# Performance work log

Measured on AMD Instinct MI355X. Metric: run time of the kernel, lower is better.

## Reference

```python
import math
import jax, jax.numpy as jnp
import numpy as np

EMBED_DIM = 1024
NUM_HEADS = 16
HEAD_DIM = EMBED_DIM // NUM_HEADS
ROTARY_DIM = HEAD_DIM  # default: rotary_dim = head_dim
BASE = 10000.0


def _rope_cos_sin(seq_len, d, dtype=jnp.float32):
    # theta: [d/2], positions: [S]
    theta = 1.0 / (BASE ** (jnp.arange(0, d, 2, dtype=jnp.float32) / d))
    pos = jnp.arange(seq_len, dtype=jnp.float32)
    idx_theta = pos[:, None] * theta[None, :]          # [S, d/2]
    idx_theta2 = jnp.concatenate([idx_theta, idx_theta], axis=-1)  # [S, d]
    return jnp.cos(idx_theta2).astype(dtype), jnp.sin(idx_theta2).astype(dtype)


def _apply_rope(x):
    # x: [B, H, S, head_dim]; rotate first ROTARY_DIM features
    S = x.shape[-2]
    cos, sin = _rope_cos_sin(S, ROTARY_DIM, x.dtype)   # [S, ROTARY_DIM]
    x_rope, x_pass = x[..., :ROTARY_DIM], x[..., ROTARY_DIM:]
    d2 = ROTARY_DIM // 2
    neg_half = jnp.concatenate([-x_rope[..., d2:], x_rope[..., :d2]], axis=-1)
    x_rope = x_rope * cos + neg_half * sin
    return jnp.concatenate([x_rope, x_pass], axis=-1)


def setup_inputs() -> dict:
    key = jax.random.key(0)
    ks = jax.random.split(key, 9)
    B, S, E = 4, 2048, EMBED_DIM
    scale = 1.0 / math.sqrt(E)
    inp = {
        "x": jax.random.normal(ks[0], (B, S, E), dtype=jnp.float32),
        "attn_mask": jnp.ones((B, S), dtype=jnp.int32),
        "Wq": jax.random.normal(ks[1], (E, E), dtype=jnp.float32) * scale,
        "bq": jnp.zeros((E,), dtype=jnp.float32),
        "Wk": jax.random.normal(ks[2], (E, E), dtype=jnp.float32) * scale,
        "bk": jnp.zeros((E,), dtype=jnp.float32),
        "Wv": jax.random.normal(ks[3], (E, E), dtype=jnp.float32) * scale,
        "bv": jnp.zeros((E,), dtype=jnp.float32),
        "Wo": jax.random.normal(ks[4], (E, E), dtype=jnp.float32) * scale,
        "bo": jnp.zeros((E,), dtype=jnp.float32),
    }
    return inp


def reference(x, attn_mask, Wq, bq, Wk, bk, Wv, bv, Wo, bo):
    B, S, E = x.shape
    H, D = NUM_HEADS, HEAD_DIM

    def proj(W, b):
        # [B,S,E] -> [B,H,S,D]
        y = jnp.einsum('bse,ef->bsf', x, W) + b
        return y.reshape(B, S, H, D).transpose(0, 2, 1, 3)

    q = _apply_rope(proj(Wq, bq))
    k = _apply_rope(proj(Wk, bk))
    v = proj(Wv, bv)

    scores = jnp.einsum('bhsd,bhtd->bhst', q, k) / math.sqrt(D)  # [B,H,S,S]
    mask = attn_mask[:, None, None, :]  # [B,1,1,S]
    scores = jnp.where(mask == 0, jnp.float32(-1e9).astype(scores.dtype), scores)
    attn = jax.nn.softmax(scores, axis=-1)
    out = jnp.einsum('bhst,bhtd->bhsd', attn, v)  # [B,H,S,D]
    out = out.transpose(0, 2, 1, 3).reshape(B, S, E)
    return jnp.einsum('bse,ef->bsf', out, Wo) + bo
```

## Files before the change

kernel.cpp:

```cpp
#include <hip/hip_runtime.h>
#include <math.h>

typedef __attribute__((ext_vector_type(8))) short short8;
typedef __attribute__((ext_vector_type(4))) float f32x4;
typedef __attribute__((ext_vector_type(4))) unsigned short us4;
typedef __attribute__((ext_vector_type(4))) unsigned int u32x4;
typedef __attribute__((ext_vector_type(4))) int i32x4;
typedef unsigned short u16;
typedef unsigned int u32;

#define LOG2E 1.4426950408889634f

static __device__ __forceinline__ u16 f2bf(float f){
  u32 u = __builtin_bit_cast(u32, f);
  u = (u + 0x7FFFu + ((u >> 16) & 1u)) >> 16;
  return (u16)u;
}

static __device__ __forceinline__ void gload16(const void* g, void* l){
  __builtin_amdgcn_global_load_lds((const __attribute__((address_space(1))) void*)g,
                                   (__attribute__((address_space(3))) void*)l,
                                   16, 0, 0);
}

static __device__ __forceinline__ f32x4 mfma16(short8 a, short8 b, f32x4 c){
  return __builtin_amdgcn_mfma_f32_16x16x32_bf16(a, b, c, 0, 0, 0);
}

__global__ void rope_tab_k(float* __restrict__ cosT, float* __restrict__ sinT){
  int idx = blockIdx.x * 256 + threadIdx.x;
  int s = idx >> 5, i = idx & 31;
  double th = pow(10000.0, -((double)(2 * i)) / 64.0);
  float ang = (float)s * (float)th;
  cosT[idx] = (float)cos((double)ang);
  sinT[idx] = (float)sin((double)ang);
}

__global__ void cvt_x_k(const float* __restrict__ x, u16* __restrict__ xb, int n){
  int i = (blockIdx.x * 256 + threadIdx.x) * 4;
  if (i >= n) return;
  f32x4 v = *(const f32x4*)(x + i);
  us4 o; o[0]=f2bf(v[0]); o[1]=f2bf(v[1]); o[2]=f2bf(v[2]); o[3]=f2bf(v[3]);
  *(us4*)(xb + i) = o;
}

__global__ void wt_cvt_k(const float* __restrict__ W0, const float* __restrict__ W1,
                         const float* __restrict__ W2, const float* __restrict__ W3,
                         u16* __restrict__ out){
  __shared__ float t[32][33];
  const float* W = (blockIdx.z == 0) ? W0 : (blockIdx.z == 1) ? W1 : (blockIdx.z == 2) ? W2 : W3;
  u16* O = out + (size_t)blockIdx.z * 1024 * 1024;
  int tx = threadIdx.x, ty = threadIdx.y;
  int kb = blockIdx.y * 32, nb = blockIdx.x * 32;
  #pragma unroll
  for (int i = 0; i < 4; i++)
    t[ty + i*8][tx] = W[(size_t)(kb + ty + i*8) * 1024 + nb + tx];
  __syncthreads();
  #pragma unroll
  for (int i = 0; i < 4; i++)
    O[(size_t)(nb + ty + i*8) * 1024 + kb + tx] = f2bf(t[tx][ty + i*8]);
}

__global__ __launch_bounds__(256, 2)
void qkv_gemm_k(const u16* __restrict__ A, const u16* __restrict__ WT,
                const float* __restrict__ bq, const float* __restrict__ bk,
                const float* __restrict__ bv,
                const float* __restrict__ cosT, const float* __restrict__ sinT,
                u16* __restrict__ Qr, u16* __restrict__ Kr, u16* __restrict__ Vt)
{
  __shared__ __align__(16) u16 Al[128][64];
  __shared__ __align__(16) u16 Bl[128][64];
  const int mode = blockIdx.y >> 3;
  const int cy   = blockIdx.y & 7;
  const u16* BT = WT + (size_t)mode * 1024 * 1024;
  const float* bias = (mode == 0) ? bq : (mode == 1) ? bk : bv;
  u16* outB = (mode == 0) ? Qr : (mode == 1) ? Kr : Vt;

  const int tid = threadIdx.x;
  const int w = tid >> 6, lane = tid & 63, g = lane >> 4, c = lane & 15;
  const int wr = w >> 1, wc = w & 1;
  const int R0 = blockIdx.x * 128, C0 = cy * 128;

  f32x4 acc[4][4];
  const f32x4 vz = {0.f, 0.f, 0.f, 0.f};
  #pragma unroll
  for (int mi = 0; mi < 4; mi++)
    #pragma unroll
    for (int ni = 0; ni < 4; ni++) acc[mi][ni] = vz;

  const u16* gA[4]; const u16* gB[4]; u16* lA[4]; u16* lB[4];
  #pragma unroll
  for (int i = 0; i < 4; i++){
    int I = w * 4 + i;
    int rr = I * 8 + (lane >> 3), kk = (lane & 7) * 8;
    gA[i] = A  + (size_t)(R0 + rr) * 1024 + kk;
    gB[i] = BT + (size_t)(C0 + rr) * 1024 + kk;
    lA[i] = &Al[I * 8][0];
    lB[i] = &Bl[I * 8][0];
  }

  for (int t = 0; t < 16; ++t){
    const int k0 = t * 64;
    #pragma unroll
    for (int i = 0; i < 4; i++){
      gload16(gA[i] + k0, lA[i]);
      gload16(gB[i] + k0, lB[i]);
    }
    __syncthreads();
    #pragma unroll
    for (int ki = 0; ki < 2; ++ki){
      short8 af[4], bfr[4];
      #pragma unroll
      for (int mi = 0; mi < 4; mi++) af[mi]  = *(const short8*)&Al[wr*64 + mi*16 + c][ki*32 + g*8];
      #pragma unroll
      for (int ni = 0; ni < 4; ni++) bfr[ni] = *(const short8*)&Bl[wc*64 + ni*16 + c][ki*32 + g*8];
      #pragma unroll
      for (int mi = 0; mi < 4; mi++)
        #pragma unroll
        for (int ni = 0; ni < 4; ni++)
          acc[mi][ni] = mfma16(af[mi], bfr[ni], acc[mi][ni]);
    }
    __syncthreads();
  }

  if (mode == 2){
    int h = cy * 2 + wc;
    #pragma unroll
    for (int ni = 0; ni < 4; ni++){
      int col = C0 + wc*64 + ni*16 + c;
      int d = ni*16 + c;
      float bvv = bias[col];
      #pragma unroll
      for (int mi = 0; mi < 4; mi++){
        int row0 = R0 + wr*64 + mi*16 + g*4;
        int b = row0 >> 11, s0 = row0 & 2047;
        us4 pk;
        #pragma unroll
        for (int r = 0; r < 4; r++) pk[r] = f2bf(acc[mi][ni][r] + bvv);
        *(us4*)&outB[((size_t)(b*16 + h)*64 + d)*2048 + s0] = pk;
      }
    }
  } else {
    int h = cy * 2 + wc;
    const float qs = (mode == 0) ? 0.125f : 1.0f;
    float bvv[4];
    #pragma unroll
    for (int ni = 0; ni < 4; ni++) bvv[ni] = bias[C0 + wc*64 + ni*16 + c];
    #pragma unroll
    for (int mi = 0; mi < 4; mi++){
      int row0 = R0 + wr*64 + mi*16 + g*4;
      int b = row0 >> 11;
      #pragma unroll
      for (int r = 0; r < 4; r++){
        int s = (row0 + r) & 2047;
        float v0 = acc[mi][0][r] + bvv[0];
        float v1 = acc[mi][1][r] + bvv[1];
        float v2 = acc[mi][2][r] + bvv[2];
        float v3 = acc[mi][3][r] + bvv[3];
        float ca = cosT[s*32 + c],      sa = sinT[s*32 + c];
        float cb = cosT[s*32 + 16 + c], sb = sinT[s*32 + 16 + c];
        float o0 = (v0*ca - v2*sa) * qs, o2 = (v2*ca + v0*sa) * qs;
        float o1 = (v1*cb - v3*sb) * qs, o3 = (v3*cb + v1*sb) * qs;
        size_t base = ((size_t)(b*16 + h)*2048 + s)*64;
        outB[base +  0 + c] = f2bf(o0);
        outB[base + 16 + c] = f2bf(o1);
        outB[base + 32 + c] = f2bf(o2);
        outB[base + 48 + c] = f2bf(o3);
      }
    }
  }
}

__global__ __launch_bounds__(256, 2)
void out_gemm_k(const u16* __restrict__ A, const u16* __restrict__ BT,
                const float* __restrict__ bias, float* __restrict__ outF)
{
  __shared__ __align__(16) u16 Al[128][64];
  __shared__ __align__(16) u16 Bl[128][64];
  const int tid = threadIdx.x;
  const int w = tid >> 6, lane = tid & 63, g = lane >> 4, c = lane & 15;
  const int wr = w >> 1, wc = w & 1;
  const int R0 = blockIdx.x * 128, C0 = blockIdx.y * 128;

  f32x4 acc[4][4];
  const f32x4 vz = {0.f, 0.f, 0.f, 0.f};
  #pragma unroll
  for (int mi = 0; mi < 4; mi++)
    #pragma unroll
    for (int ni = 0; ni < 4; ni++) acc[mi][ni] = vz;

  const u16* gA[4]; const u16* gB[4]; u16* lA[4]; u16* lB[4];
  #pragma unroll
  for (int i = 0; i < 4; i++){
    int I = w * 4 + i;
    int rr = I * 8 + (lane >> 3), kk = (lane & 7) * 8;
    gA[i] = A  + (size_t)(R0 + rr) * 1024 + kk;
    gB[i] = BT + (size_t)(C0 + rr) * 1024 + kk;
    lA[i] = &Al[I * 8][0];
    lB[i] = &Bl[I * 8][0];
  }

  for (int t = 0; t < 16; ++t){
    const int k0 = t * 64;
    #pragma unroll
    for (int i = 0; i < 4; i++){
      gload16(gA[i] + k0, lA[i]);
      gload16(gB[i] + k0, lB[i]);
    }
    __syncthreads();
    #pragma unroll
    for (int ki = 0; ki < 2; ++ki){
      short8 af[4], bfr[4];
      #pragma unroll
      for (int mi = 0; mi < 4; mi++) af[mi]  = *(const short8*)&Al[wr*64 + mi*16 + c][ki*32 + g*8];
      #pragma unroll
      for (int ni = 0; ni < 4; ni++) bfr[ni] = *(const short8*)&Bl[wc*64 + ni*16 + c][ki*32 + g*8];
      #pragma unroll
      for (int mi = 0; mi < 4; mi++)
        #pragma unroll
        for (int ni = 0; ni < 4; ni++)
          acc[mi][ni] = mfma16(af[mi], bfr[ni], acc[mi][ni]);
    }
    __syncthreads();
  }

  #pragma unroll
  for (int mi = 0; mi < 4; mi++){
    #pragma unroll
    for (int ni = 0; ni < 4; ni++){
      int col = C0 + wc*64 + ni*16 + c;
      float bvv = bias[col];
      int row0 = R0 + wr*64 + mi*16 + g*4;
      #pragma unroll
      for (int r = 0; r < 4; r++)
        outF[(size_t)(row0 + r) * 1024 + col] = acc[mi][ni][r] + bvv;
    }
  }
}

__global__ __launch_bounds__(512, 4)
void attn_fwd_k(const u16* __restrict__ Q, const u16* __restrict__ K, const u16* __restrict__ V,
                const int* __restrict__ msk, u16* __restrict__ AO)
{
  __shared__ __align__(16) u16 Kl[4][64][64];
  __shared__ __align__(16) u16 Vl[4][64][64];
  __shared__ __align__(8) unsigned char Ml[2048];
  const int tid = threadIdx.x;
  const int w = tid >> 6, lane = tid & 63, g = lane >> 4, c = lane & 15;

  const int lin = blockIdx.y * 8 + blockIdx.x;
  const int v_  = (lin & 7) * 64 + (lin >> 3);
  const int bh = v_ >> 3, b = bh >> 4, h = bh & 15;
  const int qw = (v_ & 7) * 256 + w * 32;

  {
    const int* mp = msk + b*2048 + tid*4;
    i32x4 a = *(const i32x4*)mp;
    u32 lo = (a[0] ? 1u : 0u) | (a[1] ? 0x100u : 0u) | (a[2] ? 0x10000u : 0u) | (a[3] ? 0x1000000u : 0u);
    *(u32*)&Ml[tid*4] = lo;
  }
  asm volatile("s_waitcnt lgkmcnt(0)" ::: "memory");

  short8 qb[2][2];
  #pragma unroll
  for (int mq = 0; mq < 2; mq++)
    #pragma unroll
    for (int ki = 0; ki < 2; ki++)
      qb[mq][ki] = *(const short8*)&Q[((size_t)bh*2048 + qw + mq*16 + c)*64 + ki*32 + g*8];

  const int l3 = lane >> 3, l7 = lane & 7;
  const int scol = (l7 ^ l3) * 8;
  const int s8 = w*8 + l3;
  const int ps = (s8 & 0x20) | ((s8 & 0x10) >> 2) | ((s8 & 0x0C) << 1) | (s8 & 3);
  const u16* gK = K + ((size_t)bh*2048 + ps)*64 + scol;
  const u16* gV = V + ((size_t)bh*64 + s8)*2048 + scol;

  gload16(gK,                       &Kl[0][w*8][0]);
  gload16(gV,                       &Vl[0][w*8][0]);
  gload16(gK + (size_t)64*64,       &Kl[1][w*8][0]);
  gload16(gV + (size_t)64,          &Vl[1][w*8][0]);

  f32x4 oacc[2][4];
  float mrun[2], lrun[2];
  const f32x4 vz = {0.f, 0.f, 0.f, 0.f};
  #pragma unroll
  for (int mq = 0; mq < 2; mq++){
    #pragma unroll
    for (int nd = 0; nd < 4; nd++) oacc[mq][nd] = vz;
    mrun[mq] = -1e30f; lrun[mq] = 0.f;
  }

  const int cs0 = (g*8) ^ ((c & 7) << 3);
  const int cs1 = (32 + g*8) ^ ((c & 7) << 3);

  for (int t = 0; t < 32; ++t){
    gload16(gK + (size_t)(t+2) * 64 * 64, &Kl[(t+2)&3][w*8][0]);
    gload16(gV + (size_t)(t+2) * 64,      &Vl[(t+2)&3][w*8][0]);
    asm volatile("s_waitcnt vmcnt(4)" ::: "memory");
    __builtin_amdgcn_s_barrier();
    asm volatile("" ::: "memory");

    const u16* Kb = &Kl[t&3][0][0];
    const u16* Vb = &Vl[t&3][0][0];
    const int t0 = t * 64;

    f32x4 sacc[4][2];
    #pragma unroll
    for (int nt = 0; nt < 4; nt++){ sacc[nt][0] = vz; sacc[nt][1] = vz; }
    #pragma unroll
    for (int ki = 0; ki < 2; ki++){
      const int cs = ki ? cs1 : cs0;
      short8 ka[4];
      #pragma unroll
      for (int nt = 0; nt < 4; nt++) ka[nt] = *(const short8*)&Kb[(nt*16 + c)*64 + cs];
      __builtin_amdgcn_s_setprio(1);
      #pragma unroll
      for (int nt = 0; nt < 4; nt++)
        #pragma unroll
        for (int mq = 0; mq < 2; mq++)
          sacc[nt][mq] = mfma16(ka[nt], qb[mq][ki], sacc[nt][mq]);
      __builtin_amdgcn_s_setprio(0);
    }

    {
      const u32 mw0 = *(const u32*)&Ml[t0 + 8*g];
      const u32 mw1 = *(const u32*)&Ml[t0 + 8*g + 4];
      const u32 mw2 = *(const u32*)&Ml[t0 + 32 + 8*g];
      const u32 mw3 = *(const u32*)&Ml[t0 + 32 + 8*g + 4];
      if (!__all((mw0 & mw1 & mw2 & mw3) == 0x01010101u)){
        const u32 mw[4] = {mw0, mw1, mw2, mw3};
        #pragma unroll
        for (int nt = 0; nt < 4; nt++)
          #pragma unroll
          for (int r = 0; r < 4; r++)
            if (((mw[nt] >> (8*r)) & 0xFFu) == 0){ sacc[nt][0][r] = -1e9f; sacc[nt][1][r] = -1e9f; }
      }
    }

    float pm[2];
    #pragma unroll
    for (int mq = 0; mq < 2; mq++){
      float a0 = fmaxf(fmaxf(sacc[0][mq][0], sacc[0][mq][1]), fmaxf(sacc[0][mq][2], sacc[0][mq][3]));
      float a1 = fmaxf(fmaxf(sacc[1][mq][0], sacc[1][mq][1]), fmaxf(sacc[1][mq][2], sacc[1][mq][3]));
      float a2 = fmaxf(fmaxf(sacc[2][mq][0], sacc[2][mq][1]), fmaxf(sacc[2][mq][2], sacc[2][mq][3]));
      float a3 = fmaxf(fmaxf(sacc[3][mq][0], sacc[3][mq][1]), fmaxf(sacc[3][mq][2], sacc[3][mq][3]));
      float mm = fmaxf(fmaxf(a0, a1), fmaxf(a2, a3));
      mm = fmaxf(mm, __shfl_xor(mm, 16, 64));
      mm = fmaxf(mm, __shfl_xor(mm, 32, 64));
      pm[mq] = mm;
    }

    if (__any((pm[0] > mrun[0] + 8.f) | (pm[1] > mrun[1] + 8.f))){
      float al[2];
      #pragma unroll
      for (int mq = 0; mq < 2; mq++){
        float mn = fmaxf(mrun[mq], pm[mq]);
        al[mq] = exp2f((mrun[mq] - mn) * LOG2E);
        mrun[mq] = mn;
        lrun[mq] *= al[mq];
      }
      #pragma unroll
      for (int mq = 0; mq < 2; mq++){
        float b0 = __shfl(al[mq], g*4 + 0, 64);
        float b1 = __shfl(al[mq], g*4 + 1, 64);
        float b2 = __shfl(al[mq], g*4 + 2, 64);
        float b3 = __shfl(al[mq], g*4 + 3, 64);
        #pragma unroll
        for (int nd = 0; nd < 4; nd++){
          oacc[mq][nd][0] *= b0; oacc[mq][nd][1] *= b1;
          oacc[mq][nd][2] *= b2; oacc[mq][nd][3] *= b3;
        }
      }
    }

    short8 pa[2][2];
    #pragma unroll
    for (int mq = 0; mq < 2; mq++){
      const float nm = -mrun[mq] * LOG2E;
      float p[16]; u32 rb[16];
      #pragma unroll
      for (int nt = 0; nt < 4; nt++)
        #pragma unroll
        for (int r = 0; r < 4; r++){
          float pp = exp2f(fmaf(sacc[nt][mq][r], LOG2E, nm));
          p[nt*4 + r] = pp;
          u32 u = __builtin_bit_cast(u32, pp);
          rb[nt*4 + r] = u + 0x7FFFu + ((u >> 16) & 1u);
        }
      float s0 = (p[0] + p[1]) + (p[2] + p[3]);
      float s1 = (p[4] + p[5]) + (p[6] + p[7]);
      float s2 = (p[8] + p[9]) + (p[10] + p[11]);
      float s3 = (p[12] + p[13]) + (p[14] + p[15]);
      lrun[mq] += (s0 + s1) + (s2 + s3);
      u32x4 q0 = { __builtin_amdgcn_perm(rb[1],  rb[0],  0x07060302u),
                   __builtin_amdgcn_perm(rb[3],  rb[2],  0x07060302u),
                   __builtin_amdgcn_perm(rb[5],  rb[4],  0x07060302u),
                   __builtin_amdgcn_perm(rb[7],  rb[6],  0x07060302u) };
      u32x4 q1 = { __builtin_amdgcn_perm(rb[9],  rb[8],  0x07060302u),
                   __builtin_amdgcn_perm(rb[11], rb[10], 0x07060302u),
                   __builtin_amdgcn_perm(rb[13], rb[12], 0x07060302u),
                   __builtin_amdgcn_perm(rb[15], rb[14], 0x07060302u) };
      pa[mq][0] = __builtin_bit_cast(short8, q0);
      pa[mq][1] = __builtin_bit_cast(short8, q1);
    }

    #pragma unroll
    for (int ki = 0; ki < 2; ki++){
      const int cs = ki ? cs1 : cs0;
      short8 va[4];
      #pragma unroll
      for (int nd = 0; nd < 4; nd++) va[nd] = *(const short8*)&Vb[(nd*16 + c)*64 + cs];
      __builtin_amdgcn_s_setprio(1);
      #pragma unroll
      for (int mq = 0; mq < 2; mq++)
        #pragma unroll
        for (int nd = 0; nd < 4; nd++)
          oacc[mq][nd] = mfma16(pa[mq][ki], va[nd], oacc[mq][nd]);
      __builtin_amdgcn_s_setprio(0);
    }
  }

  #pragma unroll
  for (int mq = 0; mq < 2; mq++){
    lrun[mq] += __shfl_xor(lrun[mq], 16, 64);
    lrun[mq] += __shfl_xor(lrun[mq], 32, 64);
    #pragma unroll
    for (int r = 0; r < 4; r++){
      float li = __shfl(lrun[mq], g*4 + r, 64);
      float inv = 1.0f / li;
      int q = qw + mq*16 + g*4 + r;
      size_t base = ((size_t)b*2048 + q)*1024 + h*64;
      #pragma unroll
      for (int nd = 0; nd < 4; nd++)
        AO[base + nd*16 + c] = f2bf(oacc[mq][nd][r] * inv);
    }
  }
}

extern "C" void kernel_launch(void* const* d_in, const int* in_sizes, int n_in,
                              void* d_out, int out_size, void* d_ws, size_t ws_size,
                              hipStream_t stream)
{
  const float* x  = (const float*)d_in[0];
  const int* mask = (const int*)d_in[1];
  const float* Wq = (const float*)d_in[2];
  const float* bq = (const float*)d_in[3];
  const float* Wk = (const float*)d_in[4];
  const float* bk = (const float*)d_in[5];
  const float* Wv = (const float*)d_in[6];
  const float* bv = (const float*)d_in[7];
  const float* Wo = (const float*)d_in[8];
  const float* bo = (const float*)d_in[9];
  float* out = (float*)d_out;
  (void)in_sizes; (void)n_in; (void)out_size; (void)ws_size;

  char* ws = (char*)d_ws;
  size_t off = 0;
  auto alloc = [&](size_t bytes){ void* p = ws + off; off += (bytes + 255) & ~(size_t)255; return p; };
  u16* xb    = (u16*)alloc((size_t)8192 * 1024 * 2);
  u16* WT    = (u16*)alloc((size_t)4 * 1024 * 1024 * 2);
  float* cosT = (float*)alloc((size_t)2048 * 32 * 4);
  float* sinT = (float*)alloc((size_t)2048 * 32 * 4);
  u16* Qr    = (u16*)alloc((size_t)8192 * 1024 * 2);
  u16* Kr    = (u16*)alloc((size_t)8192 * 1024 * 2);
  u16* Vt    = (u16*)alloc((size_t)8192 * 1024 * 2);
  u16* AO    = (u16*)alloc((size_t)8192 * 1024 * 2);

  rope_tab_k<<<dim3(256), dim3(256), 0, stream>>>(cosT, sinT);
  cvt_x_k<<<dim3(8192), dim3(256), 0, stream>>>(x, xb, 8192 * 1024);
  wt_cvt_k<<<dim3(32, 32, 4), dim3(32, 8), 0, stream>>>(Wq, Wk, Wv, Wo, WT);

  qkv_gemm_k<<<dim3(64, 24), dim3(256), 0, stream>>>(xb, WT, bq, bk, bv, cosT, sinT, Qr, Kr, Vt);

  attn_fwd_k<<<dim3(8, 64), dim3(512), 0, stream>>>(Qr, Kr, Vt, mask, AO);

  out_gemm_k<<<dim3(64, 8), dim3(256), 0, stream>>>(AO, WT + 3*1024*1024, bo, out);
}
```

Measured before the change: 242.9 us.

## Rewrite QKV GEMM as 256x256 persistent 8-wave kernel with double-buffered LDS

Replaces the 128x128 single-buffered QKV projection GEMM with a 512-thread, 8-wave kernel computing 256x256 tiles over a persistent grid of 256 blocks. Global-to-LDS loads are double-buffered and interleaved with MFMA phases, using explicit vmcnt waits, barriers and s_setprio, and LDS columns are XOR-swizzled to reduce bank conflicts. The goal is to hide load latency and raise arithmetic intensity per block. The costs are 128KB of LDS per block and larger accumulator register pressure. The 384 tiles do not divide evenly over 256 blocks, so half the blocks do a second tile and the last wave is imbalanced.

```diff
diff --git a/kernel.cpp b/kernel.cpp
--- a/kernel.cpp
+++ b/kernel.cpp
@@ -61,114 +61,157 @@
     O[(size_t)(nb + ty + i*8) * 1024 + kb + tx] = f2bf(t[tx][ty + i*8]);
 }
 
-__global__ __launch_bounds__(256, 2)
-void qkv_gemm_k(const u16* __restrict__ A, const u16* __restrict__ WT,
-                const float* __restrict__ bq, const float* __restrict__ bk,
-                const float* __restrict__ bv,
-                const float* __restrict__ cosT, const float* __restrict__ sinT,
-                u16* __restrict__ Qr, u16* __restrict__ Kr, u16* __restrict__ Vt)
+__global__ __launch_bounds__(512, 2)
+void qkv_gemm8_k(const u16* __restrict__ A, const u16* __restrict__ WT,
+                 const float* __restrict__ bq, const float* __restrict__ bk,
+                 const float* __restrict__ bv,
+                 const float* __restrict__ cosT, const float* __restrict__ sinT,
+                 u16* __restrict__ Qr, u16* __restrict__ Kr, u16* __restrict__ Vt)
 {
-  __shared__ __align__(16) u16 Al[128][64];
-  __shared__ __align__(16) u16 Bl[128][64];
-  const int mode = blockIdx.y >> 3;
-  const int cy   = blockIdx.y & 7;
-  const u16* BT = WT + (size_t)mode * 1024 * 1024;
-  const float* bias = (mode == 0) ? bq : (mode == 1) ? bk : bv;
-  u16* outB = (mode == 0) ? Qr : (mode == 1) ? Kr : Vt;
-
+  __shared__ __align__(16) u16 Al[2][256][64];
+  __shared__ __align__(16) u16 Bl[2][256][64];
   const int tid = threadIdx.x;
   const int w = tid >> 6, lane = tid & 63, g = lane >> 4, c = lane & 15;
-  const int wr = w >> 1, wc = w & 1;
-  const int R0 = blockIdx.x * 128, C0 = cy * 128;
-
-  f32x4 acc[4][4];
-  const f32x4 vz = {0.f, 0.f, 0.f, 0.f};
-  #pragma unroll
-  for (int mi = 0; mi < 4; mi++)
-    #pragma unroll
-    for (int ni = 0; ni < 4; ni++) acc[mi][ni] = vz;
-
-  const u16* gA[4]; const u16* gB[4]; u16* lA[4]; u16* lB[4];
-  #pragma unroll
-  for (int i = 0; i < 4; i++){
-    int I = w * 4 + i;
-    int rr = I * 8 + (lane >> 3), kk = (lane & 7) * 8;
-    gA[i] = A  + (size_t)(R0 + rr) * 1024 + kk;
-    gB[i] = BT + (size_t)(C0 + rr) * 1024 + kk;
-    lA[i] = &Al[I * 8][0];
-    lB[i] = &Bl[I * 8][0];
-  }
-
-  for (int t = 0; t < 16; ++t){
-    const int k0 = t * 64;
-    #pragma unroll
-    for (int i = 0; i < 4; i++){
-      gload16(gA[i] + k0, lA[i]);
-      gload16(gB[i] + k0, lB[i]);
-    }
-    __syncthreads();
-    #pragma unroll
-    for (int ki = 0; ki < 2; ++ki){
-      short8 af[4], bfr[4];
-      #pragma unroll
-      for (int mi = 0; mi < 4; mi++) af[mi]  = *(const short8*)&Al[wr*64 + mi*16 + c][ki*32 + g*8];
-      #pragma unroll
-      for (int ni = 0; ni < 4; ni++) bfr[ni] = *(const short8*)&Bl[wc*64 + ni*16 + c][ki*32 + g*8];
-      #pragma unroll
-      for (int mi = 0; mi < 4; mi++)
-        #pragma unroll
-        for (int ni = 0; ni < 4; ni++)
-          acc[mi][ni] = mfma16(af[mi], bfr[ni], acc[mi][ni]);
-    }
-    __syncthreads();
-  }
-
-  if (mode == 2){
-    int h = cy * 2 + wc;
-    #pragma unroll
-    for (int ni = 0; ni < 4; ni++){
-      int col = C0 + wc*64 + ni*16 + c;
-      int d = ni*16 + c;
-      float bvv = bias[col];
-      #pragma unroll
-      for (int mi = 0; mi < 4; mi++){
-        int row0 = R0 + wr*64 + mi*16 + g*4;
-        int b = row0 >> 11, s0 = row0 & 2047;
-        us4 pk;
-        #pragma unroll
-        for (int r = 0; r < 4; r++) pk[r] = f2bf(acc[mi][ni][r] + bvv);
-        *(us4*)&outB[((size_t)(b*16 + h)*64 + d)*2048 + s0] = pk;
+  const int wm = w >> 2, wn = w & 3;
+  const int l3 = lane >> 3, l7 = lane & 7;
+  const int cswz = ((c >> 2) & 1) << 4;
+
+#define STAGE_A(KT, H) do{ int kt_ = (KT); if (kt_ <= 15){ \
+    _Pragma("unroll") for (int j = 0; j < 2; j++){ \
+      int ib = w*16 + j*8; \
+      int rT = ((ib>>6)<<7) + (H)*64 + (ib & 63); \
+      int row = rT + l3; \
+      int ce = (l7*8) ^ (((row>>2)&1) << 4); \
+      gload16(A + (size_t)(R0 + row)*1024 + kt_*64 + ce, &Al[kt_&1][rT][0]); \
+    }}}while(0)
+
+#define STAGE_B(KT, H) do{ int kt_ = (KT); if (kt_ <= 15){ \
+    _Pragma("unroll") for (int j = 0; j < 2; j++){ \
+      int ib = w*16 + j*8; \
+      int rT = ((ib>>5)<<6) + (H)*32 + (ib & 31); \
+      int row = rT + l3; \
+      int ce = (l7*8) ^ (((row>>2)&1) << 4); \
+      gload16(BT + (size_t)(C0 + row)*1024 + kt_*64 + ce, &Bl[kt_&1][rT][0]); \
+    }}}while(0)
+
+#define RD_A(MH, BUF) do{ _Pragma("unroll") for (int mi = 0; mi < 4; mi++) \
+    _Pragma("unroll") for (int ki = 0; ki < 2; ki++) \
+      af[mi][ki] = *(const short8*)&Al[BUF][wm*128 + (MH)*64 + mi*16 + c][(ki*32 + g*8) ^ cswz]; }while(0)
+
+#define RD_B(DST, NH, BUF) do{ _Pragma("unroll") for (int ni = 0; ni < 2; ni++) \
+    _Pragma("unroll") for (int ki = 0; ki < 2; ki++) \
+      DST[ni][ki] = *(const short8*)&Bl[BUF][wn*64 + (NH)*32 + ni*16 + c][(ki*32 + g*8) ^ cswz]; }while(0)
+
+#define MM(MH, NH, BSRC) do{ __builtin_amdgcn_s_setprio(1); \
+    _Pragma("unroll") for (int ki = 0; ki < 2; ki++) \
+      _Pragma("unroll") for (int mi = 0; mi < 4; mi++) \
+        _Pragma("unroll") for (int ni = 0; ni < 2; ni++) \
+          acc[(MH)*4+mi][(NH)*2+ni] = mfma16(af[mi][ki], BSRC[ni][ki], acc[(MH)*4+mi][(NH)*2+ni]); \
+    __builtin_amdgcn_s_setprio(0); }while(0)
+
+#define BAR() do{ asm volatile("" ::: "memory"); __builtin_amdgcn_s_barrier(); asm volatile("" ::: "memory"); }while(0)
+
+  for (int tile = blockIdx.x; tile < 384; tile += 256){
+    const int rowT = tile & 31, colT = tile >> 5;
+    const int mode = colT >> 2, cy = colT & 3;
+    const int R0 = rowT * 256;
+    const int C0 = cy * 256;
+    const u16* BT = WT + (size_t)mode * 1024 * 1024;
+    const float* bias = (mode == 0) ? bq : (mode == 1) ? bk : bv;
+
+    f32x4 acc[8][4];
+    const f32x4 vz = {0.f, 0.f, 0.f, 0.f};
+    #pragma unroll
+    for (int m = 0; m < 8; m++)
+      #pragma unroll
+      for (int n = 0; n < 4; n++) acc[m][n] = vz;
+
+    short8 af[4][2], bf0[2][2], bf1[2][2];
+
+    STAGE_A(0, 0); STAGE_B(0, 0); STAGE_B(0, 1); STAGE_A(0, 1);
+    STAGE_A(1, 0); STAGE_B(1, 0); STAGE_B(1, 1);
+    asm volatile("s_waitcnt vmcnt(6)" ::: "memory");
+    BAR();
+
+    for (int it = 0; it < 8; ++it){
+      const int T = it * 2;
+      RD_A(0, 0); RD_B(bf0, 0, 0); STAGE_A(T+1, 1);
+      BAR(); MM(0, 0, bf0); BAR();
+      RD_B(bf1, 1, 0); STAGE_A(T+2, 0);
+      BAR(); MM(0, 1, bf1); BAR();
+      RD_A(1, 0); STAGE_B(T+2, 0);
+      BAR(); MM(1, 1, bf1); BAR();
+      STAGE_B(T+2, 1);
+      BAR(); MM(1, 0, bf0);
+      if (it < 7) asm volatile("s_waitcnt vmcnt(6)" ::: "memory");
+      else        asm volatile("s_waitcnt vmcnt(0)" ::: "memory");
+      BAR();
+      RD_A(0, 1); RD_B(bf0, 0, 1); STAGE_A(T+2, 1);
+      BAR(); MM(0, 0, bf0); BAR();
+      RD_B(bf1, 1, 1); STAGE_A(T+3, 0);
+      BAR(); MM(0, 1, bf1); BAR();
+      RD_A(1, 1); STAGE_B(T+3, 0);
+      BAR(); MM(1, 1, bf1); BAR();
+      STAGE_B(T+3, 1);
+      BAR(); MM(1, 0, bf0);
+      if (it < 7) asm volatile("s_waitcnt vmcnt(6)" ::: "memory");
+      else        asm volatile("s_waitcnt vmcnt(0)" ::: "memory");
+      BAR();
+    }
+
+    const int h = cy * 4 + wn;
+    if (mode == 2){
+      #pragma unroll
+      for (int n = 0; n < 4; n++){
+        int d = n*16 + c;
+        float bvv = bias[C0 + wn*64 + n*16 + c];
+        #pragma unroll
+        for (int m = 0; m < 8; m++){
+          int row0 = R0 + wm*128 + m*16 + g*4;
+          int b = row0 >> 11, s0 = row0 & 2047;
+          us4 pk;
+          #pragma unroll
+          for (int r = 0; r < 4; r++) pk[r] = f2bf(acc[m][n][r] + bvv);
+          *(us4*)&Vt[((size_t)(b*16 + h)*64 + d)*2048 + s0] = pk;
+        }
       }
-    }
-  } else {
-    int h = cy * 2 + wc;
-    const float qs = (mode == 0) ? 0.125f : 1.0f;
-    float bvv[4];
-    #pragma unroll
-    for (int ni = 0; ni < 4; ni++) bvv[ni] = bias[C0 + wc*64 + ni*16 + c];
-    #pragma unroll
-    for (int mi = 0; mi < 4; mi++){
-      int row0 = R0 + wr*64 + mi*16 + g*4;
-      int b = row0 >> 11;
-      #pragma unroll
-      for (int r = 0; r < 4; r++){
-        int s = (row0 + r) & 2047;
-        float v0 = acc[mi][0][r] + bvv[0];
-        float v1 = acc[mi][1][r] + bvv[1];
-        float v2 = acc[mi][2][r] + bvv[2];
-        float v3 = acc[mi][3][r] + bvv[3];
-        float ca = cosT[s*32 + c],      sa = sinT[s*32 + c];
-        float cb = cosT[s*32 + 16 + c], sb = sinT[s*32 + 16 + c];
-        float o0 = (v0*ca - v2*sa) * qs, o2 = (v2*ca + v0*sa) * qs;
-        float o1 = (v1*cb - v3*sb) * qs, o3 = (v3*cb + v1*sb) * qs;
-        size_t base = ((size_t)(b*16 + h)*2048 + s)*64;
-        outB[base +  0 + c] = f2bf(o0);
-        outB[base + 16 + c] = f2bf(o1);
-        outB[base + 32 + c] = f2bf(o2);
-        outB[base + 48 + c] = f2bf(o3);
+    } else {
+      u16* outB = (mode == 0) ? Qr : Kr;
+      const float qs = (mode == 0) ? 0.125f : 1.0f;
+      float bvv[4];
+      #pragma unroll
+      for (int n = 0; n < 4; n++) bvv[n] = bias[C0 + wn*64 + n*16 + c];
+      #pragma unroll
+      for (int m = 0; m < 8; m++){
+        int row0 = R0 + wm*128 + m*16 + g*4;
+        int b = row0 >> 11;
+        #pragma unroll
+        for (int r = 0; r < 4; r++){
+          int s = (row0 + r) & 2047;
+          float v0 = acc[m][0][r] + bvv[0];
+          float v1 = acc[m][1][r] + bvv[1];
+          float v2 = acc[m][2][r] + bvv[2];
+          float v3 = acc[m][3][r] + bvv[3];
+          float ca = cosT[s*32 + c],      sa = sinT[s*32 + c];
+          float cb = cosT[s*32 + 16 + c], sb = sinT[s*32 + 16 + c];
+          float o0 = (v0*ca - v2*sa) * qs, o2 = (v2*ca + v0*sa) * qs;
+          float o1 = (v1*cb - v3*sb) * qs, o3 = (v3*cb + v1*sb) * qs;
+          size_t base = ((size_t)(b*16 + h)*2048 + s)*64;
+          outB[base +  0 + c] = f2bf(o0);
+          outB[base + 16 + c] = f2bf(o1);
+          outB[base + 32 + c] = f2bf(o2);
+          outB[base + 48 + c] = f2bf(o3);
+        }
       }
     }
-  }
+    BAR();
+  }
+#undef STAGE_A
+#undef STAGE_B
+#undef RD_A
+#undef RD_B
+#undef MM
+#undef BAR
 }
 
 __global__ __launch_bounds__(256, 2)
@@ -470,7 +513,7 @@
   cvt_x_k<<<dim3(8192), dim3(256), 0, stream>>>(x, xb, 8192 * 1024);
   wt_cvt_k<<<dim3(32, 32, 4), dim3(32, 8), 0, stream>>>(Wq, Wk, Wv, Wo, WT);
 
-  qkv_gemm_k<<<dim3(64, 24), dim3(256), 0, stream>>>(xb, WT, bq, bk, bv, cosT, sinT, Qr, Kr, Vt);
+  qkv_gemm8_k<<<dim3(256), dim3(512), 0, stream>>>(xb, WT, bq, bk, bv, cosT, sinT, Qr, Kr, Vt);
 
   attn_fwd_k<<<dim3(8, 64), dim3(512), 0, stream>>>(Qr, Kr, Vt, mask, AO);
 
```

After: 264.6 us. 8.9% more time.
